# Optimization experiments

Hardware: AMD Instinct MI355X
Metric: run time of the kernel (lower is better)

Reference implementation:

```python
import jax, jax.numpy as jnp
import numpy as np

N = 100000        # nodes
E = 3200000       # edges (avg degree 32)
D_IN, D_H, D_OUT = 128, 128, 64
EPS = 1e-5        # BatchNorm eps


def setup_inputs() -> dict:
    key = jax.random.key(0)
    ks = jax.random.split(key, 12)
    s = 0.1
    return {
        "x": jax.random.normal(ks[0], (N, D_IN), jnp.float32),
        "edge_index": jax.random.randint(ks[1], (2, E), 0, N, jnp.int32),
        "W1": jax.random.normal(ks[2], (D_IN, D_H), jnp.float32) * s,
        "b1": jnp.zeros((D_H,), jnp.float32),
        "W2": jax.random.normal(ks[3], (D_H, D_H), jnp.float32) * s,
        "b2": jnp.zeros((D_H,), jnp.float32),
        "W3": jax.random.normal(ks[4], (D_H, D_OUT), jnp.float32) * s,
        "b3": jnp.zeros((D_OUT,), jnp.float32),
        "g1": jnp.ones((D_H,), jnp.float32),
        "be1": jnp.zeros((D_H,), jnp.float32),
        "g2": jnp.ones((D_H,), jnp.float32),
        "be2": jnp.zeros((D_H,), jnp.float32),
    }


def reference(x, edge_index, W1, b1, W2, b2, W3, b3, g1, be1, g2, be2):
    # GCNConv normalization: add self-loops, symmetric deg^-1/2 A deg^-1/2
    loop = jnp.arange(N, dtype=edge_index.dtype)
    src = jnp.concatenate([edge_index[0], loop])   # [E+N]
    dst = jnp.concatenate([edge_index[1], loop])   # [E+N]
    deg = jax.ops.segment_sum(jnp.ones(src.shape, x.dtype), dst, num_segments=N)
    dinv = jnp.where(deg > 0, jax.lax.rsqrt(deg), 0.0)
    norm = (dinv[src] * dinv[dst])[:, None]        # [E+N, 1]

    def conv(h, W, b):
        h = h @ W                                   # dense transform [N, d]
        msg = h[src] * norm                         # gather + scale [E+N, d]
        return jax.ops.segment_sum(msg, dst, num_segments=N) + b

    def bn(h, g, be):  # BatchNorm1d over nodes (batch stats, eval-style dropout)
        m = h.mean(axis=0)
        v = h.var(axis=0)
        return (h - m) * jax.lax.rsqrt(v + EPS) * g + be

    h = jax.nn.relu(bn(conv(x, W1, b1), g1, be1))
    h = jax.nn.relu(bn(conv(h, W2, b2), g2, be2))
    h = conv(h, W3, b3)
    return jax.nn.softmax(h, axis=1)
```

## Files before the change

kernel.cpp:

```cpp
#include <hip/hip_runtime.h>
#include <hip/hip_fp16.h>

constexpr int   NN   = 100000;
constexpr int   NE   = 3200000;
constexpr float BN_EPS = 1e-5f;

constexpr int MG_B  = (NN / 32 + 3) / 4;
constexpr int NB    = (NN + 127) / 128;
constexpr int HB    = 256;
constexpr int CHUNK = NE / HB;
constexpr int BKT_CAP = 5120;

typedef _Float16 half8 __attribute__((ext_vector_type(8)));
typedef float    floatx16 __attribute__((ext_vector_type(16)));
typedef float    floatx8  __attribute__((ext_vector_type(8)));

__global__ __launch_bounds__(256) void k_wprep_all(const float* __restrict__ W1,
                                                   const float* __restrict__ W2,
                                                   const float* __restrict__ W3,
                                                   _Float16* __restrict__ Wt1,
                                                   _Float16* __restrict__ Wt2,
                                                   _Float16* __restrict__ Wt3) {
  int idx = blockIdx.x * 256 + threadIdx.x;
  if (idx < 16384) {
    int k = idx >> 7, n = idx & 127;
    Wt1[n * 128 + k] = (_Float16)W1[idx];
  } else if (idx < 32768) {
    int j = idx - 16384, k = j >> 7, n = j & 127;
    Wt2[n * 128 + k] = (_Float16)W2[j];
  } else if (idx < 40960) {
    int j = idx - 32768, k = j >> 6, n = j & 63;
    Wt3[n * 128 + k] = (_Float16)W3[j];
  }
}

__global__ __launch_bounds__(256) void k_f1(const int* __restrict__ dst,
                                            int* __restrict__ blkhist,
                                            const float* __restrict__ x,
                                            const _Float16* __restrict__ Wt1,
                                            _Float16* __restrict__ C) {
  __shared__ int h[NB];
  if (blockIdx.x < MG_B) {
    int wid  = (blockIdx.x * 256 + threadIdx.x) >> 6;
    int lane = threadIdx.x & 63;
    if (wid >= NN / 32) return;
    const int m = lane & 31;
    const int q = lane >> 5;
    const int row0 = wid * 32;
    const float* Arow = x + (size_t)(row0 + m) * 128 + q * 8;

    floatx16 acc[4] = {};
#pragma unroll
    for (int s = 0; s < 8; ++s) {
      float4 a0 = *(const float4*)(Arow + 16 * s);
      float4 a1 = *(const float4*)(Arow + 16 * s + 4);
      half8 af;
      af[0] = (_Float16)a0.x; af[1] = (_Float16)a0.y;
      af[2] = (_Float16)a0.z; af[3] = (_Float16)a0.w;
      af[4] = (_Float16)a1.x; af[5] = (_Float16)a1.y;
      af[6] = (_Float16)a1.z; af[7] = (_Float16)a1.w;
#pragma unroll
      for (int ct = 0; ct < 4; ++ct) {
        half8 bf = *(const half8*)(Wt1 + (size_t)(ct * 32 + m) * 128 + q * 8 + 16 * s);
        acc[ct] = __builtin_amdgcn_mfma_f32_32x32x16_f16(af, bf, acc[ct], 0, 0, 0);
      }
    }
#pragma unroll
    for (int ct = 0; ct < 4; ++ct)
#pragma unroll
      for (int r = 0; r < 16; ++r) {
        int row = (r & 3) + 8 * (r >> 2) + 4 * q;
        C[(size_t)(row0 + row) * 128 + ct * 32 + m] = (_Float16)acc[ct][r];
      }
  } else {
    int j = blockIdx.x - MG_B;
    int t = threadIdx.x;
    for (int b = t; b < NB; b += 256) h[b] = 0;
    __syncthreads();
    int base = j * CHUNK;
    for (int e = base + t; e < base + CHUNK; e += 256)
      atomicAdd(&h[dst[e] >> 7], 1);
    __syncthreads();
    for (int b = t; b < NB; b += 256) blkhist[j * NB + b] = h[b];
  }
}

__global__ __launch_bounds__(256) void k_scan_bkt_a(const int* __restrict__ blkhist,
                                                    int* __restrict__ blkbase,
                                                    int* __restrict__ total) {
  int wid  = (blockIdx.x * 256 + threadIdx.x) >> 6;
  int lane = threadIdx.x & 63;
  if (wid >= NB) return;
  int i0 = lane * 4;
  int v0 = blkhist[(i0 + 0) * NB + wid];
  int v1 = blkhist[(i0 + 1) * NB + wid];
  int v2 = blkhist[(i0 + 2) * NB + wid];
  int v3 = blkhist[(i0 + 3) * NB + wid];
  int lt = v0 + v1 + v2 + v3;
  int inc = lt;
#pragma unroll
  for (int off = 1; off < 64; off <<= 1) {
    int xx = __shfl_up(inc, off);
    if (lane >= off) inc += xx;
  }
  int exc = inc - lt;
  blkbase[(i0 + 0) * NB + wid] = exc;
  blkbase[(i0 + 1) * NB + wid] = exc + v0;
  blkbase[(i0 + 2) * NB + wid] = exc + v0 + v1;
  blkbase[(i0 + 3) * NB + wid] = exc + v0 + v1 + v2;
  if (lane == 63) total[wid] = inc;
}

__global__ __launch_bounds__(1024) void k_scan_bkt_b(const int* __restrict__ total,
                                                     int* __restrict__ bbase) {
  __shared__ int s[1024];
  int t = threadIdx.x;
  int v = (t < NB) ? total[t] : 0;
  s[t] = v;
  __syncthreads();
  for (int off = 1; off < 1024; off <<= 1) {
    int xx = (t >= off) ? s[t - off] : 0;
    __syncthreads();
    s[t] += xx;
    __syncthreads();
  }
  if (t < NB) bbase[t] = s[t] - v;
  if (t == NB - 1) bbase[NB] = s[t];
}

__global__ __launch_bounds__(256) void k_scatter(const int* __restrict__ ei,
                                                 const int* __restrict__ bbase,
                                                 const int* __restrict__ blkbase,
                                                 int* __restrict__ ebuf) {
  __shared__ int cur[NB];
  int i = blockIdx.x;
  int t = threadIdx.x;
  for (int b = t; b < NB; b += 256) cur[b] = bbase[b] + blkbase[i * NB + b];
  __syncthreads();
  int base = i * CHUNK;
  for (int e = base + t; e < base + CHUNK; e += 256) {
    int s = ei[e];
    int d = ei[NE + e];
    int b = d >> 7;
    int pos = atomicAdd(&cur[b], 1);
    ebuf[pos] = s | ((d & 127) << 17);
  }
}

__global__ __launch_bounds__(256) void k_bucket(const int* __restrict__ bbase,
                                                const int* __restrict__ ebuf,
                                                int* __restrict__ rowptr,
                                                float* __restrict__ dinv,
                                                int* __restrict__ csrc) {
  __shared__ int degL[128];
  __shared__ int sc[128];
  __shared__ int curL[128];
  __shared__ int sorted[BKT_CAP];
  int b = blockIdx.x;
  int t = threadIdx.x;
  int e0 = bbase[b], e1 = bbase[b + 1];
  int cnt = e1 - e0;
  if (t < 128) degL[t] = 0;
  __syncthreads();
  for (int e = e0 + t; e < e1; e += 256)
    atomicAdd(&degL[ebuf[e] >> 17], 1);
  __syncthreads();
  if (t < 128) sc[t] = degL[t];
  __syncthreads();
  for (int off = 1; off < 128; off <<= 1) {
    int xx = 0;
    if (t < 128 && t >= off) xx = sc[t - off];
    __syncthreads();
    if (t < 128) sc[t] += xx;
    __syncthreads();
  }
  if (t < 128) {
    int node = b * 128 + t;
    if (node < NN) {
      int d = degL[t];
      int exc = sc[t] - d;
      rowptr[node] = e0 + exc;
      dinv[node] = rsqrtf((float)(d + 1));
      curL[t] = exc;
    }
  }
  if (b == NB - 1 && t == 0) rowptr[NN] = NE;
  __syncthreads();
  if (cnt <= BKT_CAP) {
    for (int e = e0 + t; e < e1; e += 256) {
      int p = ebuf[e];
      int pos = atomicAdd(&curL[p >> 17], 1);
      sorted[pos] = p & 0x1FFFF;
    }
    __syncthreads();
    for (int i = t; i < cnt; i += 256) csrc[e0 + i] = sorted[i];
  } else {
    for (int e = e0 + t; e < e1; e += 256) {
      int p = ebuf[e];
      int pos = atomicAdd(&curL[p >> 17], 1);
      csrc[e0 + pos] = p & 0x1FFFF;
    }
  }
}

template <int BN_>
__global__ __launch_bounds__(256) void k_mgemm(const _Float16* __restrict__ A,
                                               const _Float16* __restrict__ Wt,
                                               const float* __restrict__ scale,
                                               const float* __restrict__ shift,
                                               const float* __restrict__ dinv,
                                               _Float16* __restrict__ C) {
  constexpr int NCT = BN_ / 32;
  int wid  = (blockIdx.x * 256 + threadIdx.x) >> 6;
  int lane = threadIdx.x & 63;
  if (wid >= NN / 32) return;
  const int m = lane & 31;
  const int q = lane >> 5;
  const int row0 = wid * 32;

  const _Float16* Arow = A + (size_t)(row0 + m) * 128 + q * 8;

  floatx16 acc[NCT] = {};

#pragma unroll
  for (int s = 0; s < 8; ++s) {
    half8 raw = *(const half8*)(Arow + 16 * s);
    int k0 = 16 * s + q * 8;
    half8 af;
#pragma unroll
    for (int j = 0; j < 8; ++j) {
      float a = fmaxf(fmaf((float)raw[j], scale[k0 + j], shift[k0 + j]), 0.f);
      af[j] = (_Float16)a;
    }
#pragma unroll
    for (int ct = 0; ct < NCT; ++ct) {
      half8 bf = *(const half8*)(Wt + (size_t)(ct * 32 + m) * 128 + q * 8 + 16 * s);
      acc[ct] = __builtin_amdgcn_mfma_f32_32x32x16_f16(af, bf, acc[ct], 0, 0, 0);
    }
  }

#pragma unroll
  for (int ct = 0; ct < NCT; ++ct)
#pragma unroll
    for (int r = 0; r < 16; ++r) {
      int row = (r & 3) + 8 * (r >> 2) + 4 * q;
      float dv = dinv[row0 + row];
      C[(size_t)(row0 + row) * BN_ + ct * 32 + m] = (_Float16)(acc[ct][r] * dv);
    }
}

template <bool SRCSCALE>
__global__ __launch_bounds__(256) void k_agg128(const __half* __restrict__ H,
                                                const float* __restrict__ dinv,
                                                const int* __restrict__ rowptr,
                                                const int* __restrict__ srcs,
                                                __half2* __restrict__ out) {
  int wid  = (blockIdx.x * 256 + threadIdx.x) >> 6;
  int lane = threadIdx.x & 63;
  if (wid >= NN) return;
  const int g  = lane >> 4;
  const int sl = lane & 15;
  const _Float16* Hb = (const _Float16*)H + (size_t)sl * 8;
  floatx8 acc = {};
  float di = dinv[wid];
  if (g == 0) {
    half8 h = *(const half8*)(Hb + (size_t)wid * 128);
    float ds = SRCSCALE ? di : 1.f;
#pragma unroll
    for (int j = 0; j < 8; ++j) acc[j] = (float)h[j] * ds;
  }
  int beg = rowptr[wid], end = rowptr[wid + 1];
  int n = end - beg;
  int chunk = (n + 3) >> 2;
  int e  = beg + g * chunk; if (e > end) e = end;
  int ce = e + chunk;       if (ce > end) ce = end;
  for (; e + 4 <= ce; e += 4) {
    int s0 = srcs[e + 0], s1 = srcs[e + 1];
    int s2 = srcs[e + 2], s3 = srcs[e + 3];
    half8 h0 = *(const half8*)(Hb + (size_t)s0 * 128);
    half8 h1 = *(const half8*)(Hb + (size_t)s1 * 128);
    half8 h2 = *(const half8*)(Hb + (size_t)s2 * 128);
    half8 h3 = *(const half8*)(Hb + (size_t)s3 * 128);
    if (SRCSCALE) {
      float d0 = dinv[s0], d1 = dinv[s1], d2 = dinv[s2], d3 = dinv[s3];
#pragma unroll
      for (int j = 0; j < 8; ++j) {
        acc[j] = fmaf((float)h0[j], d0, acc[j]);
        acc[j] = fmaf((float)h1[j], d1, acc[j]);
        acc[j] = fmaf((float)h2[j], d2, acc[j]);
        acc[j] = fmaf((float)h3[j], d3, acc[j]);
      }
    } else {
#pragma unroll
      for (int j = 0; j < 8; ++j)
        acc[j] += ((float)h0[j] + (float)h1[j]) + ((float)h2[j] + (float)h3[j]);
    }
  }
  for (; e < ce; ++e) {
    int s0 = srcs[e];
    half8 h0 = *(const half8*)(Hb + (size_t)s0 * 128);
    float d0 = SRCSCALE ? dinv[s0] : 1.f;
#pragma unroll
    for (int j = 0; j < 8; ++j) acc[j] = fmaf((float)h0[j], d0, acc[j]);
  }
#pragma unroll
  for (int j = 0; j < 8; ++j) {
    acc[j] += __shfl_xor(acc[j], 16);
    acc[j] += __shfl_xor(acc[j], 32);
  }
  if (g == 0) {
    __half2 o[4];
#pragma unroll
    for (int j = 0; j < 4; ++j)
      o[j] = __floats2half2_rn(acc[2 * j] * di, acc[2 * j + 1] * di);
    *(int4*)(out + (size_t)wid * 64 + sl * 4) = *(const int4*)o;
  }
}

__global__ __launch_bounds__(256) void k_agg64_softmax(const __half* __restrict__ H,
                                                       const float* __restrict__ dinv,
                                                       const int* __restrict__ rowptr,
                                                       const int* __restrict__ srcs,
                                                       const float* __restrict__ b3,
                                                       float* __restrict__ out) {
  int wid  = (blockIdx.x * 256 + threadIdx.x) >> 6;
  int lane = threadIdx.x & 63;
  if (wid >= NN) return;
  const int g  = lane >> 3;
  const int sl = lane & 7;
  const _Float16* Hb = (const _Float16*)H + (size_t)sl * 8;
  floatx8 acc = {};
  if (g == 0) {
    half8 h = *(const half8*)(Hb + (size_t)wid * 64);
#pragma unroll
    for (int j = 0; j < 8; ++j) acc[j] = (float)h[j];
  }
  int beg = rowptr[wid], end = rowptr[wid + 1];
  int n = end - beg;
  int chunk = (n + 7) >> 3;
  int e  = beg + g * chunk; if (e > end) e = end;
  int ce = e + chunk;       if (ce > end) ce = end;
  for (; e + 4 <= ce; e += 4) {
    int s0 = srcs[e + 0], s1 = srcs[e + 1];
    int s2 = srcs[e + 2], s3 = srcs[e + 3];
    half8 h0 = *(const half8*)(Hb + (size_t)s0 * 64);
    half8 h1 = *(const half8*)(Hb + (size_t)s1 * 64);
    half8 h2 = *(const half8*)(Hb + (size_t)s2 * 64);
    half8 h3 = *(const half8*)(Hb + (size_t)s3 * 64);
#pragma unroll
    for (int j = 0; j < 8; ++j)
      acc[j] += ((float)h0[j] + (float)h1[j]) + ((float)h2[j] + (float)h3[j]);
  }
  for (; e < ce; ++e) {
    half8 h0 = *(const half8*)(Hb + (size_t)srcs[e] * 64);
#pragma unroll
    for (int j = 0; j < 8; ++j) acc[j] += (float)h0[j];
  }
#pragma unroll
  for (int j = 0; j < 8; ++j) {
    acc[j] += __shfl_xor(acc[j], 8);
    acc[j] += __shfl_xor(acc[j], 16);
    acc[j] += __shfl_xor(acc[j], 32);
  }
  float di = dinv[wid];
  float4 bA = *(const float4*)(b3 + sl * 8);
  float4 bB = *(const float4*)(b3 + sl * 8 + 4);
  float v[8];
  v[0] = acc[0] * di + bA.x; v[1] = acc[1] * di + bA.y;
  v[2] = acc[2] * di + bA.z; v[3] = acc[3] * di + bA.w;
  v[4] = acc[4] * di + bB.x; v[5] = acc[5] * di + bB.y;
  v[6] = acc[6] * di + bB.z; v[7] = acc[7] * di + bB.w;
  float m = v[0];
#pragma unroll
  for (int j = 1; j < 8; ++j) m = fmaxf(m, v[j]);
  m = fmaxf(m, __shfl_xor(m, 1));
  m = fmaxf(m, __shfl_xor(m, 2));
  m = fmaxf(m, __shfl_xor(m, 4));
  float s = 0.f;
#pragma unroll
  for (int j = 0; j < 8; ++j) { v[j] = __expf(v[j] - m); s += v[j]; }
  s += __shfl_xor(s, 1);
  s += __shfl_xor(s, 2);
  s += __shfl_xor(s, 4);
  float inv = 1.0f / s;
  if (g == 0) {
    float4 oA = {v[0] * inv, v[1] * inv, v[2] * inv, v[3] * inv};
    float4 oB = {v[4] * inv, v[5] * inv, v[6] * inv, v[7] * inv};
    *(float4*)(out + (size_t)wid * 64 + sl * 8)     = oA;
    *(float4*)(out + (size_t)wid * 64 + sl * 8 + 4) = oB;
  }
}

__global__ __launch_bounds__(256) void k_stats(const __half2* __restrict__ H2,
                                               float* __restrict__ S1,
                                               float* __restrict__ S2) {
  int t = threadIdx.x;
  int p = t & 63;
  int r = t >> 6;
  float2 s1 = {0.f, 0.f}, s2 = {0.f, 0.f};
  for (int row = blockIdx.x * 4 + r; row < NN; row += gridDim.x * 4) {
    float2 v = __half22float2(H2[(size_t)row * 64 + p]);
    s1.x += v.x; s1.y += v.y;
    s2.x += v.x * v.x; s2.y += v.y * v.y;
  }
  __shared__ float2 l1[256], l2[256];
  l1[t] = s1; l2[t] = s2;
  __syncthreads();
  if (t < 128) {
    l1[t].x += l1[t+128].x; l1[t].y += l1[t+128].y;
    l2[t].x += l2[t+128].x; l2[t].y += l2[t+128].y;
  }
  __syncthreads();
  if (t < 64) {
    float2 a1 = l1[t], b1 = l1[t+64];
    float2 a2 = l2[t], b2 = l2[t+64];
    atomicAdd(&S1[2*p+0], a1.x + b1.x);
    atomicAdd(&S1[2*p+1], a1.y + b1.y);
    atomicAdd(&S2[2*p+0], a2.x + b2.x);
    atomicAdd(&S2[2*p+1], a2.y + b2.y);
  }
}

__global__ void k_finalize(const float* __restrict__ S1, const float* __restrict__ S2,
                           const float* __restrict__ g,  const float* __restrict__ be,
                           float* __restrict__ scale,    float* __restrict__ shift) {
  int t = threadIdx.x;
  float mean = S1[t] * (1.0f / NN);
  float var  = S2[t] * (1.0f / NN) - mean * mean;
  float is   = rsqrtf(var + BN_EPS);
  float sc   = g[t] * is;
  scale[t] = sc;
  shift[t] = be[t] - mean * sc;
}

extern "C" void kernel_launch(void* const* d_in, const int* in_sizes, int n_in,
                              void* d_out, int out_size, void* d_ws, size_t ws_size,
                              hipStream_t stream) {
  (void)in_sizes; (void)n_in; (void)out_size; (void)ws_size;
  const float* x   = (const float*)d_in[0];
  const int*   ei  = (const int*)d_in[1];
  const float* W1  = (const float*)d_in[2];
  const float* W2  = (const float*)d_in[4];
  const float* W3  = (const float*)d_in[6];
  const float* b3  = (const float*)d_in[7];
  const float* g1  = (const float*)d_in[8];
  const float* be1 = (const float*)d_in[9];
  const float* g2  = (const float*)d_in[10];
  const float* be2 = (const float*)d_in[11];
  float* out = (float*)d_out;

  char* ws = (char*)d_ws;
  size_t off = 0;
  auto take = [&](size_t bytes) -> char* {
    char* p = ws + off;
    off = (off + bytes + 255) & ~(size_t)255;
    return p;
  };
  float* S1a    = (float*)take(128 * 4);
  float* S2a    = (float*)take(128 * 4);
  float* S1b    = (float*)take(128 * 4);
  float* S2b    = (float*)take(128 * 4);
  size_t zero_bytes = off;
  float* scale1 = (float*)take(128 * 4);
  float* shift1 = (float*)take(128 * 4);
  float* scale2 = (float*)take(128 * 4);
  float* shift2 = (float*)take(128 * 4);
  float* dinv   = (float*)take((size_t)NN * 4);
  int*   rowptr = (int*)  take((size_t)(NN + 1) * 4);
  int*   bbase  = (int*)  take((size_t)(NB + 1) * 4);
  int*   total  = (int*)  take((size_t)NB * 4);
  int*   blkhist= (int*)  take((size_t)HB * NB * 4);
  int*   blkbase= (int*)  take((size_t)HB * NB * 4);
  int*   ebuf   = (int*)  take((size_t)NE * 4);
  int*   csrc   = (int*)  take((size_t)NE * 4);
  _Float16* Wt1 = (_Float16*)take((size_t)128 * 128 * 2);
  _Float16* Wt2 = (_Float16*)take((size_t)128 * 128 * 2);
  _Float16* Wt3 = (_Float16*)take((size_t)64 * 128 * 2);
  _Float16* Hf  = (_Float16*)take((size_t)NN * 128 * 2);
  _Float16* hB  = (_Float16*)take((size_t)NN * 128 * 2);

  (void)hipMemsetAsync(d_ws, 0, zero_bytes, stream);

  const int mgB  = MG_B;
  const int aggB = (NN + 3) / 4;
  const int scanAB = (NB + 3) / 4;

  k_wprep_all<<<160, 256, 0, stream>>>(W1, W2, W3, Wt1, Wt2, Wt3);

  k_f1<<<MG_B + HB, 256, 0, stream>>>(ei + NE, blkhist, x, Wt1, Hf);

  k_scan_bkt_a<<<scanAB, 256, 0, stream>>>(blkhist, blkbase, total);
  k_scan_bkt_b<<<1, 1024, 0, stream>>>(total, bbase);
  k_scatter<<<HB, 256, 0, stream>>>(ei, bbase, blkbase, ebuf);
  k_bucket<<<NB, 256, 0, stream>>>(bbase, ebuf, rowptr, dinv, csrc);

  k_agg128<true><<<aggB, 256, 0, stream>>>((const __half*)Hf, dinv, rowptr, csrc, (__half2*)hB);
  k_stats<<<1024, 256, 0, stream>>>((const __half2*)hB, S1a, S2a);
  k_finalize<<<1, 128, 0, stream>>>(S1a, S2a, g1, be1, scale1, shift1);

  k_mgemm<128><<<mgB, 256, 0, stream>>>(hB, Wt2, scale1, shift1, dinv, Hf);
  k_agg128<false><<<aggB, 256, 0, stream>>>((const __half*)Hf, dinv, rowptr, csrc, (__half2*)hB);
  k_stats<<<1024, 256, 0, stream>>>((const __half2*)hB, S1b, S2b);
  k_finalize<<<1, 128, 0, stream>>>(S1b, S2b, g2, be2, scale2, shift2);

  k_mgemm<64><<<mgB, 256, 0, stream>>>(hB, Wt3, scale2, shift2, dinv, Hf);
  k_agg64_softmax<<<aggB, 256, 0, stream>>>((const __half*)Hf, dinv, rowptr, csrc, b3, out);
}
```

Before: 685.9 us.

## Store 128-wide features as column panels and aggregate one panel per block

```diff
diff --git a/kernel.cpp b/kernel.cpp
--- a/kernel.cpp
+++ b/kernel.cpp
@@ -10,10 +10,14 @@
 constexpr int HB    = 256;
 constexpr int CHUNK = NE / HB;
 constexpr int BKT_CAP = 5120;
+constexpr int IDX_CAP = 1536;
+constexpr int NPAN = 8;
 
 typedef _Float16 half8 __attribute__((ext_vector_type(8)));
 typedef float    floatx16 __attribute__((ext_vector_type(16)));
 typedef float    floatx8  __attribute__((ext_vector_type(8)));
+typedef int      intx4   __attribute__((ext_vector_type(4)));
+
 
 __global__ __launch_bounds__(256) void k_wprep_all(const float* __restrict__ W1,
                                                    const float* __restrict__ W2,
@@ -66,12 +70,15 @@
       }
     }
 #pragma unroll
-    for (int ct = 0; ct < 4; ++ct)
+    for (int ct = 0; ct < 4; ++ct) {
+      int p = ct * 2 + (m >> 4);
+      int off = m & 15;
 #pragma unroll
       for (int r = 0; r < 16; ++r) {
         int row = (r & 3) + 8 * (r >> 2) + 4 * q;
-        C[(size_t)(row0 + row) * 128 + ct * 32 + m] = (_Float16)acc[ct][r];
+        C[((size_t)p * NN + row0 + row) * 16 + off] = (_Float16)acc[ct][r];
       }
+    }
   } else {
     int j = blockIdx.x - MG_B;
     int t = threadIdx.x;
@@ -151,10 +158,12 @@
                                                 const int* __restrict__ ebuf,
                                                 int* __restrict__ rowptr,
                                                 float* __restrict__ dinv,
-                                                int* __restrict__ csrc) {
+                                                int* __restrict__ csrc,
+                                                _Float16* __restrict__ Hf) {
   __shared__ int degL[128];
   __shared__ int sc[128];
   __shared__ int curL[128];
+  __shared__ float dvs[128];
   __shared__ int sorted[BKT_CAP];
   int b = blockIdx.x;
   int t = threadIdx.x;
@@ -176,13 +185,16 @@
   }
   if (t < 128) {
     int node = b * 128 + t;
+    float dv = 0.f;
     if (node < NN) {
       int d = degL[t];
       int exc = sc[t] - d;
       rowptr[node] = e0 + exc;
-      dinv[node] = rsqrtf((float)(d + 1));
+      dv = rsqrtf((float)(d + 1));
+      dinv[node] = dv;
       curL[t] = exc;
     }
+    dvs[t] = dv;
   }
   if (b == NB - 1 && t == 0) rowptr[NN] = NE;
   __syncthreads();
@@ -201,9 +213,22 @@
       csrc[e0 + pos] = p & 0x1FFFF;
     }
   }
-}
-
-template <int BN_>
+  int node = b * 128 + (t >> 1);
+  if (node < NN) {
+    float dv = dvs[t >> 1];
+    size_t base = (size_t)node * 16 + (t & 1) * 8;
+#pragma unroll
+    for (int k = 0; k < NPAN; ++k) {
+      size_t a = (size_t)k * (NN * 16) + base;
+      half8 h = *(const half8*)(Hf + a);
+#pragma unroll
+      for (int j = 0; j < 8; ++j) h[j] = (_Float16)((float)h[j] * dv);
+      *(half8*)(Hf + a) = h;
+    }
+  }
+}
+
+template <int BN_, bool POUT>
 __global__ __launch_bounds__(256) void k_mgemm(const _Float16* __restrict__ A,
                                                const _Float16* __restrict__ Wt,
                                                const float* __restrict__ scale,
@@ -218,13 +243,13 @@
   const int q = lane >> 5;
   const int row0 = wid * 32;
 
-  const _Float16* Arow = A + (size_t)(row0 + m) * 128 + q * 8;
+  const _Float16* Abase = A + (size_t)(row0 + m) * 16 + q * 8;
 
   floatx16 acc[NCT] = {};
 
 #pragma unroll
   for (int s = 0; s < 8; ++s) {
-    half8 raw = *(const half8*)(Arow + 16 * s);
+    half8 raw = *(const half8*)(Abase + (size_t)s * (NN * 16));
     int k0 = 16 * s + q * 8;
     half8 af;
 #pragma unroll
@@ -240,80 +265,85 @@
   }
 
 #pragma unroll
-  for (int ct = 0; ct < NCT; ++ct)
+  for (int ct = 0; ct < NCT; ++ct) {
+    int p = ct * 2 + (m >> 4);
+    int off = m & 15;
 #pragma unroll
     for (int r = 0; r < 16; ++r) {
       int row = (r & 3) + 8 * (r >> 2) + 4 * q;
       float dv = dinv[row0 + row];
-      C[(size_t)(row0 + row) * BN_ + ct * 32 + m] = (_Float16)(acc[ct][r] * dv);
-    }
-}
-
-template <bool SRCSCALE>
-__global__ __launch_bounds__(256) void k_agg128(const __half* __restrict__ H,
-                                                const float* __restrict__ dinv,
-                                                const int* __restrict__ rowptr,
-                                                const int* __restrict__ srcs,
-                                                __half2* __restrict__ out) {
-  int wid  = (blockIdx.x * 256 + threadIdx.x) >> 6;
-  int lane = threadIdx.x & 63;
-  if (wid >= NN) return;
-  const int g  = lane >> 4;
-  const int sl = lane & 15;
-  const _Float16* Hb = (const _Float16*)H + (size_t)sl * 8;
+      _Float16 val = (_Float16)(acc[ct][r] * dv);
+      if (POUT)
+        C[((size_t)p * NN + row0 + row) * 16 + off] = val;
+      else
+        C[(size_t)(row0 + row) * BN_ + ct * 32 + m] = val;
+    }
+  }
+}
+
+__global__ __launch_bounds__(256) void k_agg128p(const _Float16* __restrict__ Hp,
+                                                 const float* __restrict__ dinv,
+                                                 const int* __restrict__ rowptr,
+                                                 const int* __restrict__ srcs,
+                                                 _Float16* __restrict__ outp) {
+  __shared__ int sidx[4][IDX_CAP];
+  int p  = blockIdx.x & 7;
+  int nb = blockIdx.x >> 3;
+  int t  = threadIdx.x;
+  int w    = t >> 6;
+  int lane = t & 63;
+  int pr = lane >> 1;
+  int hi = lane & 1;
+  int node = nb * 128 + w * 32 + pr;
+  int nodec = node < NN ? node : NN - 1;
+  int beg = rowptr[nodec];
+  int end = rowptr[nodec + 1];
+  int w0   = __shfl(beg, 0);
+  int wend = __shfl(end, 62);
+  int cnt  = wend - w0;
+  int* my = sidx[w];
+  int scnt = cnt < IDX_CAP ? cnt : IDX_CAP;
+  for (int i = lane; i < scnt; i += 64)
+    my[i] = __builtin_nontemporal_load(srcs + w0 + i);
+
+  const _Float16* base = Hp + (size_t)p * (NN * 16) + hi * 8;
   floatx8 acc = {};
-  float di = dinv[wid];
-  if (g == 0) {
-    half8 h = *(const half8*)(Hb + (size_t)wid * 128);
-    float ds = SRCSCALE ? di : 1.f;
-#pragma unroll
-    for (int j = 0; j < 8; ++j) acc[j] = (float)h[j] * ds;
-  }
-  int beg = rowptr[wid], end = rowptr[wid + 1];
-  int n = end - beg;
-  int chunk = (n + 3) >> 2;
-  int e  = beg + g * chunk; if (e > end) e = end;
-  int ce = e + chunk;       if (ce > end) ce = end;
-  for (; e + 4 <= ce; e += 4) {
-    int s0 = srcs[e + 0], s1 = srcs[e + 1];
-    int s2 = srcs[e + 2], s3 = srcs[e + 3];
-    half8 h0 = *(const half8*)(Hb + (size_t)s0 * 128);
-    half8 h1 = *(const half8*)(Hb + (size_t)s1 * 128);
-    half8 h2 = *(const half8*)(Hb + (size_t)s2 * 128);
-    half8 h3 = *(const half8*)(Hb + (size_t)s3 * 128);
-    if (SRCSCALE) {
-      float d0 = dinv[s0], d1 = dinv[s1], d2 = dinv[s2], d3 = dinv[s3];
-#pragma unroll
-      for (int j = 0; j < 8; ++j) {
-        acc[j] = fmaf((float)h0[j], d0, acc[j]);
-        acc[j] = fmaf((float)h1[j], d1, acc[j]);
-        acc[j] = fmaf((float)h2[j], d2, acc[j]);
-        acc[j] = fmaf((float)h3[j], d3, acc[j]);
+  if (node < NN) {
+    half8 h = *(const half8*)(base + (size_t)node * 16);
+#pragma unroll
+    for (int j = 0; j < 8; ++j) acc[j] = (float)h[j];
+    int lb = beg - w0, le = end - w0;
+    int e = lb;
+    if (le <= IDX_CAP) {
+      for (; e + 4 <= le; e += 4) {
+        int s0 = my[e + 0], s1 = my[e + 1], s2 = my[e + 2], s3 = my[e + 3];
+        half8 h0 = *(const half8*)(base + (size_t)s0 * 16);
+        half8 h1 = *(const half8*)(base + (size_t)s1 * 16);
+        half8 h2 = *(const half8*)(base + (size_t)s2 * 16);
+        half8 h3 = *(const half8*)(base + (size_t)s3 * 16);
+#pragma unroll
+        for (int j = 0; j < 8; ++j)
+          acc[j] += ((float)h0[j] + (float)h1[j]) + ((float)h2[j] + (float)h3[j]);
+      }
+      for (; e < le; ++e) {
+        half8 h0 = *(const half8*)(base + (size_t)my[e] * 16);
+#pragma unroll
+        for (int j = 0; j < 8; ++j) acc[j] += (float)h0[j];
       }
     } else {
-#pragma unroll
-      for (int j = 0; j < 8; ++j)
-        acc[j] += ((float)h0[j] + (float)h1[j]) + ((float)h2[j] + (float)h3[j]);
-    }
-  }
-  for (; e < ce; ++e) {
-    int s0 = srcs[e];
-    half8 h0 = *(const half8*)(Hb + (size_t)s0 * 128);
-    float d0 = SRCSCALE ? dinv[s0] : 1.f;
-#pragma unroll
-    for (int j = 0; j < 8; ++j) acc[j] = fmaf((float)h0[j], d0, acc[j]);
-  }
-#pragma unroll
-  for (int j = 0; j < 8; ++j) {
-    acc[j] += __shfl_xor(acc[j], 16);
-    acc[j] += __shfl_xor(acc[j], 32);
-  }
-  if (g == 0) {
+      for (e = beg; e < end; ++e) {
+        half8 h0 = *(const half8*)(base + (size_t)srcs[e] * 16);
+#pragma unroll
+        for (int j = 0; j < 8; ++j) acc[j] += (float)h0[j];
+      }
+    }
+    float di = dinv[node];
     __half2 o[4];
 #pragma unroll
     for (int j = 0; j < 4; ++j)
       o[j] = __floats2half2_rn(acc[2 * j] * di, acc[2 * j + 1] * di);
-    *(int4*)(out + (size_t)wid * 64 + sl * 4) = *(const int4*)o;
+    intx4* dst = (intx4*)(outp + ((size_t)p * NN + node) * 16 + hi * 8);
+    __builtin_nontemporal_store(*(const intx4*)o, dst);
   }
 }
 
@@ -395,11 +425,12 @@
                                                float* __restrict__ S1,
                                                float* __restrict__ S2) {
   int t = threadIdx.x;
-  int p = t & 63;
+  int cp = t & 63;
   int r = t >> 6;
+  const __half2* Pb = H2 + (size_t)(cp >> 3) * (NN * 8) + (cp & 7);
   float2 s1 = {0.f, 0.f}, s2 = {0.f, 0.f};
   for (int row = blockIdx.x * 4 + r; row < NN; row += gridDim.x * 4) {
-    float2 v = __half22float2(H2[(size_t)row * 64 + p]);
+    float2 v = __half22float2(Pb[(size_t)row * 8]);
     s1.x += v.x; s1.y += v.y;
     s2.x += v.x * v.x; s2.y += v.y * v.y;
   }
@@ -414,10 +445,10 @@
   if (t < 64) {
     float2 a1 = l1[t], b1 = l1[t+64];
     float2 a2 = l2[t], b2 = l2[t+64];
-    atomicAdd(&S1[2*p+0], a1.x + b1.x);
-    atomicAdd(&S1[2*p+1], a1.y + b1.y);
-    atomicAdd(&S2[2*p+0], a2.x + b2.x);
-    atomicAdd(&S2[2*p+1], a2.y + b2.y);
+    atomicAdd(&S1[2*cp+0], a1.x + b1.x);
+    atomicAdd(&S1[2*cp+1], a1.y + b1.y);
+    atomicAdd(&S2[2*cp+0], a2.x + b2.x);
+    atomicAdd(&S2[2*cp+1], a2.y + b2.y);
   }
 }
 
@@ -483,6 +514,7 @@
 
   const int mgB  = MG_B;
   const int aggB = (NN + 3) / 4;
+  const int aggPB = NPAN * ((NN + 127) / 128);
   const int scanAB = (NB + 3) / 4;
 
   k_wprep_all<<<160, 256, 0, stream>>>(W1, W2, W3, Wt1, Wt2, Wt3);
@@ -492,17 +524,17 @@
   k_scan_bkt_a<<<scanAB, 256, 0, stream>>>(blkhist, blkbase, total);
   k_scan_bkt_b<<<1, 1024, 0, stream>>>(total, bbase);
   k_scatter<<<HB, 256, 0, stream>>>(ei, bbase, blkbase, ebuf);
-  k_bucket<<<NB, 256, 0, stream>>>(bbase, ebuf, rowptr, dinv, csrc);
-
-  k_agg128<true><<<aggB, 256, 0, stream>>>((const __half*)Hf, dinv, rowptr, csrc, (__half2*)hB);
+  k_bucket<<<NB, 256, 0, stream>>>(bbase, ebuf, rowptr, dinv, csrc, Hf);
+
+  k_agg128p<<<aggPB, 256, 0, stream>>>(Hf, dinv, rowptr, csrc, hB);
   k_stats<<<1024, 256, 0, stream>>>((const __half2*)hB, S1a, S2a);
   k_finalize<<<1, 128, 0, stream>>>(S1a, S2a, g1, be1, scale1, shift1);
 
-  k_mgemm<128><<<mgB, 256, 0, stream>>>(hB, Wt2, scale1, shift1, dinv, Hf);
-  k_agg128<false><<<aggB, 256, 0, stream>>>((const __half*)Hf, dinv, rowptr, csrc, (__half2*)hB);
+  k_mgemm<128, true><<<mgB, 256, 0, stream>>>(hB, Wt2, scale1, shift1, dinv, Hf);
+  k_agg128p<<<aggPB, 256, 0, stream>>>(Hf, dinv, rowptr, csrc, hB);
   k_stats<<<1024, 256, 0, stream>>>((const __half2*)hB, S1b, S2b);
   k_finalize<<<1, 128, 0, stream>>>(S1b, S2b, g2, be2, scale2, shift2);
 
-  k_mgemm<64><<<mgB, 256, 0, stream>>>(hB, Wt3, scale2, shift2, dinv, Hf);
+  k_mgemm<64, false><<<mgB, 256, 0, stream>>>(hB, Wt3, scale2, shift2, dinv, Hf);
   k_agg64_softmax<<<aggB, 256, 0, stream>>>((const __half*)Hf, dinv, rowptr, csrc, b3, out);
 }
```

Result: slower. 789.5 us (+15.1%).
